# Kernel tuning notes

Measured on AMD Instinct MI355X. Metric: run time of the kernel, lower is better.

Reference implementation:

```python
import jax, jax.numpy as jnp
import numpy as np

DIM = 2048
HIDDEN = 8192
EPS = 1e-6


def rms_norm(x, gamma):
    # x: [..., dim]
    var = jnp.mean(x * x, axis=-1, keepdims=True)
    return x * jax.lax.rsqrt(var + EPS) * gamma


def activation_quant(x):
    # per-token absmax int8 fake-quant
    scale = 127.0 / jnp.maximum(jnp.max(jnp.abs(x), axis=-1, keepdims=True), 1e-5)
    return jnp.clip(jnp.round(x * scale), -128.0, 127.0) / scale


def weight_quant(w):
    # per-tensor ternary (BitNet b1.58) fake-quant
    scale = 1.0 / jnp.maximum(jnp.mean(jnp.abs(w)), 1e-5)
    return jnp.clip(jnp.round(w * scale), -1.0, 1.0) / scale


def bit_linear(x, w):
    # straight-through estimator on both activations and weights
    xq = x + jax.lax.stop_gradient(activation_quant(x) - x)
    wq = w + jax.lax.stop_gradient(weight_quant(w) - w)
    # x: [b, s, in], w: [out, in] (torch Linear layout)
    return jnp.einsum('bsi,oi->bso', xq, wq)


def setup_inputs() -> dict:
    key = jax.random.key(0)
    k_x, k_w1, k_w2 = jax.random.split(key, 3)
    x = jax.random.normal(k_x, (4, 2048, DIM), dtype=jnp.float32)
    # kaiming-uniform-ish init like nn.Linear
    b1 = 1.0 / np.sqrt(DIM)
    b2 = 1.0 / np.sqrt(HIDDEN)
    w1 = jax.random.uniform(k_w1, (HIDDEN, DIM), dtype=jnp.float32, minval=-b1, maxval=b1)
    w2 = jax.random.uniform(k_w2, (DIM, HIDDEN), dtype=jnp.float32, minval=-b2, maxval=b2)
    gamma = jnp.ones((DIM,), dtype=jnp.float32)
    return {"x": x, "w1": w1, "w2": w2, "gamma": gamma}


def reference(x, w1, w2, gamma):
    h = bit_linear(rms_norm(x, gamma), w1)          # [b, s, hidden]
    h = jax.nn.gelu(h, approximate=False)           # nn.GELU default = exact erf
    return bit_linear(h, w2)                        # [b, s, dim]
```

## Files before the change

kernel.cpp:

```cpp
#include <hip/hip_runtime.h>
#include <cstdint>
#include <cstddef>

#define D_DIM 2048
#define D_HID 8192
#define N_TOK 8192

typedef int v4i __attribute__((ext_vector_type(4)));
typedef float v4f __attribute__((ext_vector_type(4)));
typedef _Float16 v8h __attribute__((ext_vector_type(8)));

__device__ __forceinline__ void gload16(const void* g, void* l) {
  __builtin_amdgcn_global_load_lds(
      (__attribute__((address_space(1))) void*)(void*)(const_cast<void*>(g)),
      (__attribute__((address_space(3))) void*)(void*)(l), 16, 0, 0);
}

__device__ __forceinline__ unsigned pack4i8(int a, int b, int c, int d) {
  return (unsigned)(a & 255) | ((unsigned)(b & 255) << 8) |
         ((unsigned)(c & 255) << 16) | ((unsigned)(d & 255) << 24);
}

__device__ __forceinline__ int clampi(int v, int lo, int hi) {
  return v < lo ? lo : (v > hi ? hi : v);
}

__device__ __forceinline__ float gelu_fast(float c) {
  const float ax = fabsf(c) * 0.70710678118654752440f;
  const float t = 1.0f / fmaf(0.3275911f, ax, 1.0f);
  const float poly =
      t * fmaf(t, fmaf(t, fmaf(t, fmaf(t, 1.061405429f, -1.453152027f),
                               1.421413741f), -0.284496736f), 0.254829592f);
  const float e = 1.0f - poly * __expf(-ax * ax);
  const float es = copysignf(e, c);
  return 0.5f * c * (1.0f + es);
}

__global__ __launch_bounds__(256) void wsum_k(const float* __restrict__ w1,
                                              const float* __restrict__ w2,
                                              double* __restrict__ part) {
  const int b = blockIdx.x;
  const float* w = (b < 1024) ? w1 : w2;
  const size_t base = (size_t)(b & 1023) * 16384;
  const int t = threadIdx.x;
  double s = 0.0;
  for (int i = 0; i < 64; ++i) s += fabs((double)w[base + (size_t)i * 256 + t]);
  __shared__ double red[256];
  red[t] = s;
  __syncthreads();
  for (int st = 128; st; st >>= 1) {
    if (t < st) red[t] += red[t + st];
    __syncthreads();
  }
  if (!t) part[b] = red[0];
}

__global__ __launch_bounds__(256) void wfinal_k(const double* __restrict__ part,
                                                double* __restrict__ swd,
                                                float* __restrict__ wsc) {
  __shared__ double red[256];
  const int t = threadIdx.x;
  for (int m = 0; m < 2; ++m) {
    double s = part[m * 1024 + t] + part[m * 1024 + 256 + t] +
               part[m * 1024 + 512 + t] + part[m * 1024 + 768 + t];
    red[t] = s;
    __syncthreads();
    for (int st = 128; st; st >>= 1) {
      if (t < st) red[t] += red[t + st];
      __syncthreads();
    }
    if (!t) {
      double mean = red[0] / 16777216.0;
      double m2 = fmax(mean, 1e-5);
      swd[m] = 1.0 / m2;
      wsc[m] = (float)m2;
    }
    __syncthreads();
  }
}

__global__ __launch_bounds__(256) void wquant_k(const float* __restrict__ w,
                                                int8_t* __restrict__ q,
                                                const double* __restrict__ swd, int idx) {
  const double s = swd[idx];
  const size_t i = ((size_t)blockIdx.x * 256 + threadIdx.x) * 4;
  const float4 v = *(const float4*)&w[i];
  const int q0 = clampi((int)__builtin_rint((double)v.x * s), -1, 1);
  const int q1 = clampi((int)__builtin_rint((double)v.y * s), -1, 1);
  const int q2 = clampi((int)__builtin_rint((double)v.z * s), -1, 1);
  const int q3 = clampi((int)__builtin_rint((double)v.w * s), -1, 1);
  *(unsigned*)&q[i] = pack4i8(q0, q1, q2, q3);
}

__global__ __launch_bounds__(256) void rmsq_k(const float* __restrict__ x,
                                              const float* __restrict__ gamma,
                                              int8_t* __restrict__ qx,
                                              float* __restrict__ sxinv) {
  const int row = blockIdx.x, t = threadIdx.x;
  const float* xr = x + (size_t)row * D_DIM;
  const v4f v0 = __builtin_nontemporal_load((const v4f*)&xr[t * 4]);
  const v4f v1 = __builtin_nontemporal_load((const v4f*)&xr[1024 + t * 4]);
  double xs[8] = {v0[0], v0[1], v0[2], v0[3], v1[0], v1[1], v1[2], v1[3]};
  double ssq = 0.0;
#pragma unroll
  for (int j = 0; j < 8; ++j) ssq += xs[j] * xs[j];
  __shared__ double red[256];
  red[t] = ssq;
  __syncthreads();
  for (int st = 128; st; st >>= 1) {
    if (t < st) red[t] += red[t + st];
    __syncthreads();
  }
  const double rn = 1.0 / sqrt(red[0] / (double)D_DIM + 1e-6);
  __syncthreads();
  const float4 g0 = *(const float4*)&gamma[t * 4];
  const float4 g1 = *(const float4*)&gamma[1024 + t * 4];
  const double gs[8] = {g0.x, g0.y, g0.z, g0.w, g1.x, g1.y, g1.z, g1.w};
  double xn[8], am = 0.0;
#pragma unroll
  for (int j = 0; j < 8; ++j) {
    xn[j] = xs[j] * rn * gs[j];
    am = fmax(am, fabs(xn[j]));
  }
  red[t] = am;
  __syncthreads();
  for (int st = 128; st; st >>= 1) {
    if (t < st) red[t] = fmax(red[t], red[t + st]);
    __syncthreads();
  }
  const double amax = fmax(red[0], 1e-5);
  const double s = 127.0 / amax;
  int q[8];
#pragma unroll
  for (int j = 0; j < 8; ++j) q[j] = clampi((int)__builtin_rint(xn[j] * s), -128, 127);
  unsigned* qo = (unsigned*)(qx + (size_t)row * D_DIM);
  qo[t] = pack4i8(q[0], q[1], q[2], q[3]);
  qo[256 + t] = pack4i8(q[4], q[5], q[6], q[7]);
  if (!t) sxinv[row] = (float)(amax / 127.0);
}

__global__ __launch_bounds__(256) void hquant16_k(const _Float16* __restrict__ g16,
                                                  int8_t* __restrict__ qh,
                                                  const unsigned* __restrict__ amaxh,
                                                  float* __restrict__ shinv) {
  const int row = blockIdx.x, t = threadIdx.x;
  const _Float16* gr = g16 + (size_t)row * D_HID;
  const double am = fmax((double)__uint_as_float(amaxh[row]), 1e-5);
  const double s = 127.0 / am;
  if (!t) shinv[row] = (float)(am / 127.0);
  unsigned* qo = (unsigned*)(qh + (size_t)row * D_HID);
#pragma unroll
  for (int j = 0; j < 4; ++j) {
    const v8h v = *(const v8h*)&gr[j * 2048 + t * 8];
    int q[8];
#pragma unroll
    for (int e = 0; e < 8; ++e)
      q[e] = clampi((int)__builtin_rint((double)(float)v[e] * s), -128, 127);
    qo[j * 512 + t * 2 + 0] = pack4i8(q[0], q[1], q[2], q[3]);
    qo[j * 512 + t * 2 + 1] = pack4i8(q[4], q[5], q[6], q[7]);
  }
}

__global__ __launch_bounds__(256) void scalefix_k(const unsigned* __restrict__ amaxh,
                                                  float* __restrict__ shinv) {
  const int i = blockIdx.x * 256 + threadIdx.x;
  if (i < N_TOK)
    shinv[i] = (float)(fmax((double)__uint_as_float(amaxh[i]), 1e-5) / 127.0);
}

template <int EPI>
__global__ __launch_bounds__(256, 4) void gemm4_i8_k(const int8_t* __restrict__ A,
                                                     const int8_t* __restrict__ B, int K,
                                                     int NB_X,
                                                     float* __restrict__ Cf,
                                                     _Float16* __restrict__ Ch,
                                                     int8_t* __restrict__ Cq, int ldc,
                                                     const float* __restrict__ rowf,
                                                     const float* __restrict__ wscp,
                                                     unsigned* __restrict__ amax) {
  __shared__ __align__(16) int8_t Al[2][8192];
  __shared__ __align__(16) int8_t Bl[2][8192];
  const int tid = threadIdx.x;
  const int wave = tid >> 6, lane = tid & 63;
  const int hi = lane >> 4, lo = lane & 15;
  const int wr = (wave >> 1) * 64, wc = (wave & 1) * 64;

  const int nwg = gridDim.x;
  const int bid = blockIdx.x;
  const int lid = (bid & 7) * (nwg >> 3) + (bid >> 3);
  const int grp = lid >> 9;
  const int rem = lid & 511;
  const int by = rem >> 3;
  const int bx = (grp << 3) | (rem & 7);
  const int row0 = by * 128, col0 = bx * 128;

  const int srow = lane >> 2;
  const int skb = ((lane & 3) ^ ((lane >> 3) & 3)) * 16;
  const size_t aG0 = (size_t)(row0 + (2 * wave + 0) * 16 + srow) * K + skb;
  const size_t aG1 = (size_t)(row0 + (2 * wave + 1) * 16 + srow) * K + skb;
  const size_t bG0 = (size_t)(col0 + (2 * wave + 0) * 16 + srow) * K + skb;
  const size_t bG1 = (size_t)(col0 + (2 * wave + 1) * 16 + srow) * K + skb;
  const int ls0 = (2 * wave + 0) * 1024, ls1 = (2 * wave + 1) * 1024;
  const int NT = K >> 6;

  v4i acc[4][4];
#pragma unroll
  for (int m = 0; m < 4; ++m)
#pragma unroll
    for (int n = 0; n < 4; ++n) acc[m][n] = (v4i){0, 0, 0, 0};

  const int roff = lo * 64 + ((hi ^ ((lo >> 1) & 3)) * 16);
  const int asb = (wr >> 4);
  const int bsb = (wc >> 4);

#define STG(buf, T)                                                            \
  do {                                                                         \
    const size_t ko_ = (size_t)(T) * 64;                                       \
    gload16(A + aG0 + ko_, &Al[buf][ls0]);                                     \
    gload16(A + aG1 + ko_, &Al[buf][ls1]);                                     \
    gload16(B + bG0 + ko_, &Bl[buf][ls0]);                                     \
    gload16(B + bG1 + ko_, &Bl[buf][ls1]);                                     \
  } while (0)

  STG(0, 0);
  asm volatile("s_waitcnt vmcnt(0)" ::: "memory");
  __syncthreads();

  int buf = 0;
#pragma unroll 1
  for (int t = 0; t < NT; ++t) {
    if (t + 1 < NT) STG(buf ^ 1, t + 1);
    v4i af[4], bf[4];
#pragma unroll
    for (int m = 0; m < 4; ++m) af[m] = *(const v4i*)&Al[buf][(asb + m) * 1024 + roff];
#pragma unroll
    for (int n = 0; n < 4; ++n) bf[n] = *(const v4i*)&Bl[buf][(bsb + n) * 1024 + roff];
    __builtin_amdgcn_s_setprio(1);
#pragma unroll
    for (int m = 0; m < 4; ++m)
#pragma unroll
      for (int n = 0; n < 4; ++n)
        acc[m][n] = __builtin_amdgcn_mfma_i32_16x16x64_i8(af[m], bf[n], acc[m][n], 0, 0, 0);
    __builtin_amdgcn_s_setprio(0);
    asm volatile("s_waitcnt vmcnt(0)" ::: "memory");
    __syncthreads();
    buf ^= 1;
  }
#undef STG

  const float mw = wscp[0];
#pragma unroll
  for (int m = 0; m < 4; ++m) {
#pragma unroll
    for (int r = 0; r < 4; ++r) {
      const int grow = row0 + wr + m * 16 + hi * 4 + r;
      const float f = rowf[grow] * mw;
      if constexpr (EPI == 0 || EPI == 1 || EPI == 4) {
        float rmax = 0.f;
#pragma unroll
        for (int n = 0; n < 4; ++n) {
          const int gcol = col0 + wc + n * 16 + lo;
          const float c = (float)acc[m][n][r] * f;
          const float gv = gelu_fast(c);
          if constexpr (EPI == 1)
            __builtin_nontemporal_store(gv, &Cf[(size_t)grow * ldc + gcol]);
          if constexpr (EPI == 4)
            Ch[(size_t)grow * ldc + gcol] = (_Float16)gv;
          rmax = fmaxf(rmax, fabsf(gv));
        }
#pragma unroll
        for (int sh = 1; sh < 16; sh <<= 1) rmax = fmaxf(rmax, __shfl_xor(rmax, sh));
        if (lo == 0) atomicMax(&amax[grow], __float_as_uint(rmax));
      } else if constexpr (EPI == 3) {
        const double s = 127.0 / fmax((double)__uint_as_float(amax[grow]), 1e-5);
#pragma unroll
        for (int n = 0; n < 4; ++n) {
          const int gcol = col0 + wc + n * 16 + lo;
          const float c = (float)acc[m][n][r] * f;
          const float gv = gelu_fast(c);
          Cq[(size_t)grow * ldc + gcol] =
              (int8_t)clampi((int)__builtin_rint((double)gv * s), -128, 127);
        }
      } else {
#pragma unroll
        for (int n = 0; n < 4; ++n) {
          const int gcol = col0 + wc + n * 16 + lo;
          __builtin_nontemporal_store((float)acc[m][n][r] * f,
                                      &Cf[(size_t)grow * ldc + gcol]);
        }
      }
    }
  }
}

__global__ void fill_k(float* p, int n, float v) {
  int i = blockIdx.x * 256 + threadIdx.x;
  if (i < n) p[i] = v;
}

extern "C" void kernel_launch(void* const* d_in, const int* in_sizes, int n_in, void* d_out,
                              int out_size, void* d_ws, size_t ws_size, hipStream_t stream) {
  const float* x = (const float*)d_in[0];
  const float* w1 = (const float*)d_in[1];
  const float* w2 = (const float*)d_in[2];
  const float* gamma = (const float*)d_in[3];
  float* out = (float*)d_out;
  char* ws = (char*)d_ws;

  const size_t SQX = (size_t)N_TOK * D_DIM;
  const size_t SQW1 = (size_t)D_HID * D_DIM;
  const size_t SQW2 = (size_t)D_DIM * D_HID;
  const size_t SQH = (size_t)N_TOK * D_HID;
  const size_t SG16 = (size_t)N_TOK * D_HID * 2;

  size_t off = 0;
  int8_t* qx = (int8_t*)(ws + off);  off += SQX;
  int8_t* qw1 = (int8_t*)(ws + off); off += SQW1;
  int8_t* qw2 = (int8_t*)(ws + off); off += SQW2;
  int8_t* qh = (int8_t*)(ws + off);  off += SQH;
  float* sxinv = (float*)(ws + off);       off += (size_t)N_TOK * 4;
  unsigned* amaxh = (unsigned*)(ws + off); off += (size_t)N_TOK * 4;
  float* shinv = (float*)(ws + off);       off += (size_t)N_TOK * 4;
  double* wpart = (double*)(ws + off);     off += 2048 * 8;
  double* swd = (double*)(ws + off);       off += 2 * 8;
  float* wsc = (float*)(ws + off);         off += 2 * 4;
  off = (off + 255) & ~(size_t)255;
  const size_t needB = off;
  _Float16* g16 = (_Float16*)(ws + off);
  const size_t needA16 = off + SG16;

  if (ws_size < needB) {
    const float v = 100000.0f + (float)(ws_size >> 20);
    fill_k<<<(out_size + 255) / 256, 256, 0, stream>>>(out, out_size, v);
    return;
  }
  const bool pathA16 = (ws_size >= needA16);

  hipMemsetAsync(amaxh, 0, (size_t)N_TOK * 4, stream);
  wsum_k<<<2048, 256, 0, stream>>>(w1, w2, wpart);
  wfinal_k<<<1, 256, 0, stream>>>(wpart, swd, wsc);
  wquant_k<<<16384, 256, 0, stream>>>(w1, qw1, swd, 0);
  wquant_k<<<16384, 256, 0, stream>>>(w2, qw2, swd, 1);
  rmsq_k<<<N_TOK, 256, 0, stream>>>(x, gamma, qx, sxinv);

  const int nwg1 = (N_TOK / 128) * (D_HID / 128);
  const int nwg2 = (N_TOK / 128) * (D_DIM / 128);
  if (pathA16) {
    gemm4_i8_k<4><<<nwg1, 256, 0, stream>>>(qx, qw1, D_DIM, D_HID / 128, nullptr, g16,
                                            nullptr, D_HID, sxinv, wsc + 0, amaxh);
    hquant16_k<<<N_TOK, 256, 0, stream>>>(g16, qh, amaxh, shinv);
  } else {
    gemm4_i8_k<0><<<nwg1, 256, 0, stream>>>(qx, qw1, D_DIM, D_HID / 128, nullptr, nullptr,
                                            nullptr, D_HID, sxinv, wsc + 0, amaxh);
    scalefix_k<<<(N_TOK + 255) / 256, 256, 0, stream>>>(amaxh, shinv);
    gemm4_i8_k<3><<<nwg1, 256, 0, stream>>>(qx, qw1, D_DIM, D_HID / 128, nullptr, nullptr,
                                            qh, D_HID, sxinv, wsc + 0, amaxh);
  }
  gemm4_i8_k<2><<<nwg2, 256, 0, stream>>>(qh, qw2, D_HID, D_DIM / 128, out, nullptr,
                                          nullptr, D_DIM, shinv, wsc + 1, nullptr);
}
```

Measured before the change: 476.2 us.

## Switch int8 GEMM to 32x32x32 MFMA with new LDS layout

Replaces the 16x16x64 int8 MFMA tiling (4x4 per wave) with 32x32x32 int8 MFMAs (2x2 per wave, two k-halves per 64-wide tile). The LDS staging layout, swizzle, fragment offsets and epilogue row/column mapping are reworked to match the 32x32 output layout, with the row-max reduction widened to 32 lanes. The aim is fewer LDS fragment reads per MFMA and possibly higher MFMA throughput, at the risk of layout or bank-conflict mistakes.

```diff
diff --git a/kernel.cpp b/kernel.cpp
--- a/kernel.cpp
+++ b/kernel.cpp
@@ -7,6 +7,7 @@
 #define N_TOK 8192
 
 typedef int v4i __attribute__((ext_vector_type(4)));
+typedef int v16i __attribute__((ext_vector_type(16)));
 typedef float v4f __attribute__((ext_vector_type(4)));
 typedef _Float16 v8h __attribute__((ext_vector_type(8)));
 
@@ -182,8 +183,7 @@
   __shared__ __align__(16) int8_t Bl[2][8192];
   const int tid = threadIdx.x;
   const int wave = tid >> 6, lane = tid & 63;
-  const int hi = lane >> 4, lo = lane & 15;
-  const int wr = (wave >> 1) * 64, wc = (wave & 1) * 64;
+  const int wr = wave >> 1, wc = wave & 1;
 
   const int nwg = gridDim.x;
   const int bid = blockIdx.x;
@@ -195,23 +195,28 @@
   const int row0 = by * 128, col0 = bx * 128;
 
   const int srow = lane >> 2;
-  const int skb = ((lane & 3) ^ ((lane >> 3) & 3)) * 16;
-  const size_t aG0 = (size_t)(row0 + (2 * wave + 0) * 16 + srow) * K + skb;
-  const size_t aG1 = (size_t)(row0 + (2 * wave + 1) * 16 + srow) * K + skb;
-  const size_t bG0 = (size_t)(col0 + (2 * wave + 0) * 16 + srow) * K + skb;
-  const size_t bG1 = (size_t)(col0 + (2 * wave + 1) * 16 + srow) * K + skb;
-  const int ls0 = (2 * wave + 0) * 1024, ls1 = (2 * wave + 1) * 1024;
+  const int skb = ((lane & 3) ^ ((lane >> 2) & 3)) * 16;
+  const size_t aG0 = (size_t)(row0 + wave * 32 + srow) * K + skb;
+  const size_t aG1 = aG0 + (size_t)16 * K;
+  const size_t bG0 = (size_t)(col0 + wave * 32 + srow) * K + skb;
+  const size_t bG1 = bG0 + (size_t)16 * K;
+  const int ls0 = wave * 2048, ls1 = wave * 2048 + 1024;
   const int NT = K >> 6;
 
-  v4i acc[4][4];
-#pragma unroll
-  for (int m = 0; m < 4; ++m)
-#pragma unroll
-    for (int n = 0; n < 4; ++n) acc[m][n] = (v4i){0, 0, 0, 0};
-
-  const int roff = lo * 64 + ((hi ^ ((lo >> 1) & 3)) * 16);
-  const int asb = (wr >> 4);
-  const int bsb = (wc >> 4);
+  v16i acc[2][2];
+#pragma unroll
+  for (int mi = 0; mi < 2; ++mi)
+#pragma unroll
+    for (int ni = 0; ni < 2; ++ni)
+#pragma unroll
+      for (int e = 0; e < 16; ++e) acc[mi][ni][e] = 0;
+
+  const int arow = lane & 31;
+  const int kc = lane >> 5;
+  const int fo0 = arow * 64 + (((0 + kc) ^ (arow & 3)) * 16);
+  const int fo1 = arow * 64 + (((2 + kc) ^ (arow & 3)) * 16);
+  const int asb = wr * 2 * 2048;
+  const int bsb = wc * 2 * 2048;
 
 #define STG(buf, T)                                                            \
   do {                                                                         \
@@ -230,17 +235,23 @@
 #pragma unroll 1
   for (int t = 0; t < NT; ++t) {
     if (t + 1 < NT) STG(buf ^ 1, t + 1);
-    v4i af[4], bf[4];
-#pragma unroll
-    for (int m = 0; m < 4; ++m) af[m] = *(const v4i*)&Al[buf][(asb + m) * 1024 + roff];
-#pragma unroll
-    for (int n = 0; n < 4; ++n) bf[n] = *(const v4i*)&Bl[buf][(bsb + n) * 1024 + roff];
+    v4i a00 = *(const v4i*)&Al[buf][asb + 0 * 2048 + fo0];
+    v4i a10 = *(const v4i*)&Al[buf][asb + 1 * 2048 + fo0];
+    v4i b00 = *(const v4i*)&Bl[buf][bsb + 0 * 2048 + fo0];
+    v4i b10 = *(const v4i*)&Bl[buf][bsb + 1 * 2048 + fo0];
+    v4i a01 = *(const v4i*)&Al[buf][asb + 0 * 2048 + fo1];
+    v4i a11 = *(const v4i*)&Al[buf][asb + 1 * 2048 + fo1];
+    v4i b01 = *(const v4i*)&Bl[buf][bsb + 0 * 2048 + fo1];
+    v4i b11 = *(const v4i*)&Bl[buf][bsb + 1 * 2048 + fo1];
     __builtin_amdgcn_s_setprio(1);
-#pragma unroll
-    for (int m = 0; m < 4; ++m)
-#pragma unroll
-      for (int n = 0; n < 4; ++n)
-        acc[m][n] = __builtin_amdgcn_mfma_i32_16x16x64_i8(af[m], bf[n], acc[m][n], 0, 0, 0);
+    acc[0][0] = __builtin_amdgcn_mfma_i32_32x32x32_i8(a00, b00, acc[0][0], 0, 0, 0);
+    acc[0][1] = __builtin_amdgcn_mfma_i32_32x32x32_i8(a00, b10, acc[0][1], 0, 0, 0);
+    acc[1][0] = __builtin_amdgcn_mfma_i32_32x32x32_i8(a10, b00, acc[1][0], 0, 0, 0);
+    acc[1][1] = __builtin_amdgcn_mfma_i32_32x32x32_i8(a10, b10, acc[1][1], 0, 0, 0);
+    acc[0][0] = __builtin_amdgcn_mfma_i32_32x32x32_i8(a01, b01, acc[0][0], 0, 0, 0);
+    acc[0][1] = __builtin_amdgcn_mfma_i32_32x32x32_i8(a01, b11, acc[0][1], 0, 0, 0);
+    acc[1][0] = __builtin_amdgcn_mfma_i32_32x32x32_i8(a11, b01, acc[1][0], 0, 0, 0);
+    acc[1][1] = __builtin_amdgcn_mfma_i32_32x32x32_i8(a11, b11, acc[1][1], 0, 0, 0);
     __builtin_amdgcn_s_setprio(0);
     asm volatile("s_waitcnt vmcnt(0)" ::: "memory");
     __syncthreads();
@@ -249,18 +260,20 @@
 #undef STG
 
   const float mw = wscp[0];
-#pragma unroll
-  for (int m = 0; m < 4; ++m) {
-#pragma unroll
-    for (int r = 0; r < 4; ++r) {
-      const int grow = row0 + wr + m * 16 + hi * 4 + r;
+  const int ccol = lane & 31;
+  const int rbase = (lane >> 5) * 4;
+#pragma unroll
+  for (int mi = 0; mi < 2; ++mi) {
+#pragma unroll
+    for (int r = 0; r < 16; ++r) {
+      const int grow = row0 + wr * 64 + mi * 32 + (r & 3) + 8 * (r >> 2) + rbase;
       const float f = rowf[grow] * mw;
       if constexpr (EPI == 0 || EPI == 1 || EPI == 4) {
         float rmax = 0.f;
 #pragma unroll
-        for (int n = 0; n < 4; ++n) {
-          const int gcol = col0 + wc + n * 16 + lo;
-          const float c = (float)acc[m][n][r] * f;
+        for (int ni = 0; ni < 2; ++ni) {
+          const int gcol = col0 + wc * 64 + ni * 32 + ccol;
+          const float c = (float)acc[mi][ni][r] * f;
           const float gv = gelu_fast(c);
           if constexpr (EPI == 1)
             __builtin_nontemporal_store(gv, &Cf[(size_t)grow * ldc + gcol]);
@@ -269,23 +282,23 @@
           rmax = fmaxf(rmax, fabsf(gv));
         }
 #pragma unroll
-        for (int sh = 1; sh < 16; sh <<= 1) rmax = fmaxf(rmax, __shfl_xor(rmax, sh));
-        if (lo == 0) atomicMax(&amax[grow], __float_as_uint(rmax));
+        for (int sh = 1; sh < 32; sh <<= 1) rmax = fmaxf(rmax, __shfl_xor(rmax, sh));
+        if (ccol == 0) atomicMax(&amax[grow], __float_as_uint(rmax));
       } else if constexpr (EPI == 3) {
         const double s = 127.0 / fmax((double)__uint_as_float(amax[grow]), 1e-5);
 #pragma unroll
-        for (int n = 0; n < 4; ++n) {
-          const int gcol = col0 + wc + n * 16 + lo;
-          const float c = (float)acc[m][n][r] * f;
+        for (int ni = 0; ni < 2; ++ni) {
+          const int gcol = col0 + wc * 64 + ni * 32 + ccol;
+          const float c = (float)acc[mi][ni][r] * f;
           const float gv = gelu_fast(c);
           Cq[(size_t)grow * ldc + gcol] =
               (int8_t)clampi((int)__builtin_rint((double)gv * s), -128, 127);
         }
       } else {
 #pragma unroll
-        for (int n = 0; n < 4; ++n) {
-          const int gcol = col0 + wc + n * 16 + lo;
-          __builtin_nontemporal_store((float)acc[m][n][r] * f,
+        for (int ni = 0; ni < 2; ++ni) {
+          const int gcol = col0 + wc * 64 + ni * 32 + ccol;
+          __builtin_nontemporal_store((float)acc[mi][ni][r] * f,
                                       &Cf[(size_t)grow * ldc + gcol]);
         }
       }
```

New measurement: 604.4 us. +26.9%, slower.
